# Performance work log

Measured on AMD Instinct MI355X. Metric: run time of the kernel, lower is better.

The kernel has to match this reference:

```python
import jax, jax.numpy as jnp
import numpy as np

B, L, N, CIN = 16, 12, 2048, 3
EMB, GRAP, LAYERS, OUT = 64, 16, 3, 12
SP, TID, DIW = 16, 16, 16
M = EMB + SP + TID + DIW  # model_size = 112


def setup_inputs() -> dict:
    key = jax.random.key(0)
    ks = jax.random.split(key, 12)
    s = jnp.float32(0.02)
    return {
        "history_data": jax.random.uniform(ks[0], (B, L, N, CIN), dtype=jnp.float32),
        "adj": jax.nn.softmax(jax.random.normal(ks[1], (N, N), dtype=jnp.float32), axis=1),
        "node_emb": jax.random.normal(ks[2], (N, SP), dtype=jnp.float32) * s,
        "tid_emb": jax.random.normal(ks[3], (288, TID), dtype=jnp.float32) * s,
        "diw_emb": jax.random.normal(ks[4], (7, DIW), dtype=jnp.float32) * s,
        "W_in": jax.random.normal(ks[5], (CIN, EMB), dtype=jnp.float32) * s,
        "b_in": jnp.zeros((EMB,), jnp.float32),
        "W_pre": jax.random.normal(ks[6], (M, 4 * M), dtype=jnp.float32) * s,
        "b_pre": jnp.zeros((4 * M,), jnp.float32),
        "E_dy": jax.random.normal(ks[7], (N, GRAP), dtype=jnp.float32) * s,
        "W_dy": jax.random.normal(ks[8], (M, 4 * M), dtype=jnp.float32) * s,
        "b_dy": jnp.zeros((4 * M,), jnp.float32),
        "W_dec": jax.random.normal(ks[9], (OUT, LAYERS, M), dtype=jnp.float32) * s,
        "b_dec": jnp.zeros((OUT,), jnp.float32),
        "W_out": jax.random.normal(ks[10], (OUT, OUT), dtype=jnp.float32) * s,
        "b_out": jnp.zeros((OUT,), jnp.float32),
    }


def _run_layer(hidd_t, A, W, b):
    """Graph-conv LSTM-style recurrent layer; returns last-timestep hidden [B,N,M]."""
    def step(ct, x):  # x: [B,N,M]
        xa = jnp.einsum('bkm,nk->bnm', x, A)      # adjacency message passing
        gates = xa @ W + b                         # [B,N,4M]
        i, f, g, o = jnp.split(gates, 4, axis=-1)
        ct = jax.nn.sigmoid(f) * ct + jax.nn.sigmoid(i) * jnp.tanh(g)
        ht = jax.nn.sigmoid(o) * jnp.tanh(ct)
        return ct, ht
    ct0 = jnp.zeros(hidd_t.shape[1:], hidd_t.dtype)  # [B,N,M]
    _, hts = jax.lax.scan(step, ct0, hidd_t)
    return hts[-1]


def reference(history_data, adj, node_emb, tid_emb, diw_emb, W_in, b_in,
              W_pre, b_pre, E_dy, W_dy, b_dy, W_dec, b_dec, W_out, b_out):
    Bx, Lx = history_data.shape[0], history_data.shape[1]
    # temporal embedding indices (truncating cast, matches torch LongTensor)
    t_idx = (history_data[..., 1] * 288).astype(jnp.int32)
    d_idx = (history_data[..., 2] * 7).astype(jnp.int32)
    inp = history_data @ W_in + b_in                                   # [B,L,N,EMB]
    node = jnp.broadcast_to(node_emb, (Bx, Lx) + node_emb.shape)       # [B,L,N,SP]
    hidd = jnp.concatenate([inp, node, tid_emb[t_idx], diw_emb[d_idx]], axis=-1)  # [B,L,N,M]
    hidd_t = jnp.moveaxis(hidd, 1, 0)                                  # [L,B,N,M]
    A_dy = jax.nn.softmax(jax.nn.relu(E_dy @ E_dy.T), axis=1)          # adaptive adjacency
    outs = [_run_layer(hidd_t, adj, W_pre, b_pre)]                     # layer 0: predefined graph
    for _ in range(LAYERS - 1):
        outs.append(_run_layer(hidd_t, A_dy, W_dy, b_dy))              # layers >0: dynamic graph
    final = jnp.stack(outs, axis=1)                                    # [B,LAYERS,N,M]
    # decoder Conv2d(layer_num->out_len, kernel (1,M)) then 1x1 Conv2d
    x = jnp.einsum('bznm,ozm->bon', final, W_dec) + b_dec[None, :, None]
    x = jnp.einsum('bon,po->bpn', x, W_out) + b_out[None, :, None]
    return x  # [B,OUT,N]
```

## Files before the change

### kernel.cpp

```cpp
#include <hip/hip_runtime.h>
#include <hip/hip_bf16.h>
#include <cstdint>
#include <cstddef>

typedef float f4 __attribute__((ext_vector_type(4)));
typedef short s16x8 __attribute__((ext_vector_type(8)));
typedef short s16x4 __attribute__((ext_vector_type(4)));

#define N_NODES 2048
#define BATCH 16
#define LSEQ 12
#define MDIM 112
#define GDIM 448
#define KC 35
#define NCOLS_X 6784
#define NREAL (KC*BATCH*LSEQ)
#define XROW 7680
#define KBIG 2048
#define KL 64
#define WTB_SH (GDIM * KL)

#define GLDS16(SRC, DST)                                                        \
    __builtin_amdgcn_global_load_lds(                                           \
        (const __attribute__((address_space(1))) void*)(SRC),                   \
        (__attribute__((address_space(3))) void*)(DST), 16, 0, 0)

#define MFMA16(ACC, AV, BV) \
    ACC = __builtin_amdgcn_mfma_f32_16x16x32_bf16(AV, BV, ACC, 0, 0, 0)

__device__ __forceinline__ short bf16hi(float v) {
    union { __hip_bfloat16 h; short s; } u;
    u.h = __float2bfloat16(v);
    return u.s;
}
__device__ __forceinline__ short bf16lo(float v) {
    union { __hip_bfloat16 h; short s; } u;
    u.h = __float2bfloat16(v);
    float r = v - __bfloat162float(u.h);
    u.h = __float2bfloat16(r);
    return u.s;
}
__device__ __forceinline__ float rcpf_(float x)  { return __builtin_amdgcn_rcpf(x); }
__device__ __forceinline__ float sigf_(float x)  { return rcpf_(1.0f + __expf(-x)); }
__device__ __forceinline__ float tanhf_(float x) { return 1.0f - 2.0f * rcpf_(1.0f + __expf(2.0f * x)); }

__device__ __forceinline__ float wave_sum(float v) {
#pragma unroll
    for (int off = 32; off > 0; off >>= 1) v += __shfl_down(v, off);
    return v;
}

__global__ void adaptive_adj_kernel(const float* __restrict__ E,
                                    const float* __restrict__ node_emb,
                                    __hip_bfloat16* __restrict__ Abig,
                                    float* __restrict__ node_a,
                                    float* __restrict__ rs)
{
    __shared__ float sbuf[N_NODES];
    __shared__ float red[256];
    __shared__ float part[17][4];
    const int n = blockIdx.x;
    const int tid = threadIdx.x;
    float en[16];
#pragma unroll
    for (int i = 0; i < 16; ++i) en[i] = E[n * 16 + i];
    float lmax = -3.4e38f;
    for (int k = tid; k < N_NODES; k += 256) {
        const float* ek = E + k * 16;
        float d = 0.f;
#pragma unroll
        for (int i = 0; i < 16; ++i) d += en[i] * ek[i];
        d = fmaxf(d, 0.0f);
        sbuf[k] = d;
        lmax = fmaxf(lmax, d);
    }
    red[tid] = lmax; __syncthreads();
    for (int s = 128; s > 0; s >>= 1) {
        if (tid < s) red[tid] = fmaxf(red[tid], red[tid + s]);
        __syncthreads();
    }
    float mx = red[0];
    __syncthreads();
    float lsum = 0.f;
    for (int k = tid; k < N_NODES; k += 256) {
        float e = __expf(sbuf[k] - mx);
        sbuf[k] = e;
        lsum += e;
    }
    red[tid] = lsum; __syncthreads();
    for (int s = 128; s > 0; s >>= 1) {
        if (tid < s) red[tid] += red[tid + s];
        __syncthreads();
    }
    float rinv = rcpf_(red[0]);
    __syncthreads();

    __hip_bfloat16* arow = Abig + (size_t)(2048 + n) * KBIG;
    float p[17];
#pragma unroll
    for (int i = 0; i < 17; ++i) p[i] = 0.f;
    for (int k = tid; k < N_NODES; k += 256) {
        float a = sbuf[k] * rinv;
        arow[k] = __float2bfloat16(a);
        const float* e = node_emb + k * 16;
        p[16] += a;
#pragma unroll
        for (int i = 0; i < 16; ++i) p[i] += a * e[i];
    }
#pragma unroll
    for (int e = 0; e < 17; ++e) {
        float v = wave_sum(p[e]);
        if ((tid & 63) == 0) part[e][tid >> 6] = v;
    }
    __syncthreads();
    if (tid < 17) {
        float s = part[tid][0] + part[tid][1] + part[tid][2] + part[tid][3];
        if (tid < 16) node_a[n * 16 + tid] = s;
        else rs[n] = s;
    }
}

__global__ void node_rs_kernel(const float* __restrict__ A,
                               const float* __restrict__ node_emb,
                               float* __restrict__ node_a, float* __restrict__ rs)
{
    __shared__ float part[17][4];
    const int n = blockIdx.x;
    const int tid = threadIdx.x;
    float p[17];
#pragma unroll
    for (int i = 0; i < 17; ++i) p[i] = 0.f;
    for (int k = tid; k < N_NODES; k += 256) {
        float a = A[(size_t)n * N_NODES + k];
        const float* e = node_emb + k * 16;
        p[16] += a;
#pragma unroll
        for (int i = 0; i < 16; ++i) p[i] += a * e[i];
    }
#pragma unroll
    for (int e = 0; e < 17; ++e) {
        float v = wave_sum(p[e]);
        if ((tid & 63) == 0) part[e][tid >> 6] = v;
    }
    __syncthreads();
    if (tid < 17) {
        float s = part[tid][0] + part[tid][1] + part[tid][2] + part[tid][3];
        if (tid < 16) node_a[n * 16 + tid] = s;
        else rs[n] = s;
    }
}

__global__ void wtb_pack_kernel(const float* __restrict__ W_in,
                                const float* __restrict__ b_in,
                                const float* __restrict__ Wp,
                                const float* __restrict__ bp,
                                const float* __restrict__ Wd,
                                const float* __restrict__ bd,
                                short* __restrict__ outp)
{
    int idx = blockIdx.x * 256 + threadIdx.x;
    if (idx >= 2 * GDIM * KL) return;
    int z = idx >= GDIM * KL;
    int rem = idx - z * GDIM * KL;
    const float* W  = z ? Wd : Wp;
    const float* bg = z ? bd : bp;
    int p = rem & 63;
    int r = rem >> 6;
    int tile = r >> 4, gc = r & 15;
    int mi = tile >> 2, co = tile & 3;
    int g = co * 112 + mi * 16 + gc;

    float v = 0.f; bool lo = false; bool zero = false;
    #define DOTW(VEC) ({ float s_ = 0.f;                                     \
        for (int m = 0; m < 64; ++m) s_ += (VEC)[m] * W[(size_t)m * GDIM + g];\
        s_; })
    if (p < 3)         v = DOTW(W_in + p * 64);
    else if (p < 35)   v = W[(size_t)(80 + p - 3) * GDIM + g];
    else if (p < 38)   v = DOTW(W_in + (p - 35) * 64);
    else if (p < 41) { v = DOTW(W_in + (p - 38) * 64); lo = true; }
    else if (p == 41)  v = bg[g];
    else if (p == 42)  v = DOTW(b_in);
    else if (p < 59)   v = W[(size_t)(64 + p - 43) * GDIM + g];
    else if (p == 59) { v = bg[g]; lo = true; }
    else if (p == 60) { v = DOTW(b_in); lo = true; }
    else zero = true;
    #undef DOTW
    short s = zero ? (short)0 : (lo ? bf16lo(v) : bf16hi(v));
    int a = r * 128 + p * 2;
    int asw = a ^ (((a >> 7) & 7) << 4);
    outp[(size_t)z * WTB_SH + (asw >> 1)] = s;
}

#define AQUADS (2048 * 2048 / 4)
#define XQUADS (NCOLS_X * 2048 / 4)
__global__ void pack_build_kernel(const float* __restrict__ adj,
                                  const float* __restrict__ hist,
                                  const float* __restrict__ tid_emb,
                                  const float* __restrict__ diw_emb,
                                  __hip_bfloat16* __restrict__ Abig,
                                  __hip_bfloat16* __restrict__ XT)
{
    int idx = blockIdx.x * 256 + threadIdx.x;
    if (idx < AQUADS) {
        int e0 = idx << 2;
        int k = e0 & 2047;
        int m = e0 >> 11;
        f4 v = *(const f4*)(adj + (size_t)m * 2048 + k);
        s16x4 o = { bf16hi(v[0]), bf16hi(v[1]), bf16hi(v[2]), bf16hi(v[3]) };
        *(s16x4*)((short*)Abig + (size_t)m * KBIG + k) = o;
        return;
    }
    int xi = idx - AQUADS;
    if (xi >= XQUADS) return;
    int e0 = xi << 2;
    int k0 = e0 & 2047;
    int jl = e0 >> 11;
    s16x4 o = {0, 0, 0, 0};
    if (jl < NREAL) {
        int c = jl % KC;
        int bl = jl / KC;
#pragma unroll
        for (int i = 0; i < 4; ++i) {
            const float* h = hist + ((size_t)(bl * N_NODES + k0 + i)) * 3;
            float v;
            if (c < 3) v = h[c];
            else if (c < 19) { int ti = (int)(h[1] * 288.0f); v = tid_emb[ti * 16 + (c - 3)]; }
            else             { int di = (int)(h[2] * 7.0f);   v = diw_emb[di * 16 + (c - 19)]; }
            o[i] = bf16hi(v);
        }
    }
    *(s16x4*)((short*)XT + (size_t)jl * KBIG + k0) = o;
}

__global__ __launch_bounds__(512, 4) void gemm_bf16_kernel(const short* __restrict__ A,
                                                           const short* __restrict__ BT,
                                                           short* __restrict__ XAhi)
{
    __shared__ short As[256 * 32];
    __shared__ short Bs[128 * 32];
    const int tid = threadIdx.x;
    const int w = tid >> 6;
    const int l = tid & 63;
    const int wr = w >> 1;
    const int wc = w & 1;

    const int bid = blockIdx.y * 53 + blockIdx.x;
    const int sid = (bid & 7) * 106 + (bid >> 3);
    const int col = sid >> 4;
    const int row = sid & 15;
    const int m0 = row * 256;
    const int jt = col * 128;

    const int arow0 = tid >> 2;
    const int akc   = (tid & 3) * 8;
    const size_t gA0 = (size_t)(m0 + arow0) * KBIG + akc;
    const size_t gA1 = (size_t)(m0 + 128 + arow0) * KBIG + akc;
    const size_t gB0 = (size_t)(jt + arow0) * KBIG + akc;
    char* lA0 = (char*)As + tid * 16;
    char* lA1 = (char*)As + 8192 + tid * 16;
    char* lB0 = (char*)Bs + tid * 16;

    f4 acc[4][4];
#pragma unroll
    for (int i = 0; i < 4; ++i)
#pragma unroll
        for (int j = 0; j < 4; ++j)
#pragma unroll
            for (int e = 0; e < 4; ++e) acc[i][j][e] = 0.f;

    const int fkof = (l >> 4) * 8;

    for (int kt = 0; kt < KBIG; kt += 32) {
        __syncthreads();
        GLDS16(A  + gA0 + kt, lA0);
        GLDS16(A  + gA1 + kt, lA1);
        GLDS16(BT + gB0 + kt, lB0);
        __syncthreads();
        s16x8 a[4], b[4];
#pragma unroll
        for (int mi = 0; mi < 4; ++mi)
            a[mi] = *(const s16x8*)&As[(wr * 64 + mi * 16 + (l & 15)) * 32 + fkof];
#pragma unroll
        for (int ni = 0; ni < 4; ++ni)
            b[ni] = *(const s16x8*)&Bs[(wc * 64 + ni * 16 + (l & 15)) * 32 + fkof];
#pragma unroll
        for (int mi = 0; mi < 4; ++mi)
#pragma unroll
            for (int ni = 0; ni < 4; ++ni)
                MFMA16(acc[mi][ni], a[mi], b[ni]);
    }

    const int rbase = m0 + wr * 64 + (l >> 4) * 4;
    const int cbase = jt + wc * 64 + (l & 15);
#pragma unroll
    for (int mi = 0; mi < 4; ++mi)
#pragma unroll
        for (int ni = 0; ni < 4; ++ni) {
            int cc = cbase + ni * 16;
            if (cc < NREAL) {
                int bt = cc / KC;
                int c  = cc - bt * KC;
#pragma unroll
                for (int reg = 0; reg < 4; ++reg) {
                    size_t roff = (size_t)(rbase + mi * 16 + reg) * XROW;
                    float v = acc[mi][ni][reg];
                    XAhi[roff + (size_t)bt * 40 + c] = bf16hi(v);
                    if (c < 3) XAhi[roff + (size_t)bt * 40 + 36 + c] = bf16lo(v);
                }
            }
        }
}

__global__ __launch_bounds__(512, 4) void lstm6_kernel(
    const short* __restrict__ XAhi,
    const short* __restrict__ WtBg,
    const float* __restrict__ na_pre, const float* __restrict__ na_dy,
    const float* __restrict__ rs_pre, const float* __restrict__ rs_dy,
    float* __restrict__ H)
{
    __shared__ short sWtb[WTB_SH];
    __shared__ short sXa[128 * KL];
    const int tid = threadIdx.x;
    const int w = tid >> 6, l = tid & 63;
    const int n0 = blockIdx.x * 128;
    const int b  = blockIdx.y;
    const int z  = blockIdx.z;
    const float* na = z ? na_dy : na_pre;
    const float* rs = z ? rs_dy : rs_pre;

    {
        const char* gW = (const char*)(WtBg + (size_t)z * WTB_SH);
        char* lW = (char*)sWtb;
        for (int it = 0; it < 7; ++it) {
            int base = (it * 8 + w) * 64;
            GLDS16(gW + (size_t)(base + l) * 16, lW + base * 16);
        }
    }

    const int sr = tid & 127;
    const int pp = tid >> 7;
    const short* xarow = XAhi + (size_t)(z * 2048 + n0 + sr) * XROW;
    const float* narow = na + (size_t)(n0 + sr) * 16;
    const float rsv = rs[n0 + sr];
    char* wrow = (char*)sXa + sr * 128;
    const int wswz = (sr & 7) << 4;

    const int lm = l & 15;
    const int sm = (l & 7) << 4;
    const int kof0 = ((l >> 4) * 16) ^ sm;
    const int kof1 = (64 + (l >> 4) * 16) ^ sm;
    const int an = w * 16 + lm;
    const char* xab = (const char*)sXa;
    const char* wtbb = (const char*)sWtb;
    float* Hout = H + (size_t)z * BATCH * N_NODES * MDIM;

    float cc[7][4];
#pragma unroll
    for (int mi = 0; mi < 7; ++mi)
#pragma unroll
        for (int q = 0; q < 4; ++q) cc[mi][q] = 0.f;

    s16x8 ph0 = {0,0,0,0,0,0,0,0}, ph1 = ph0;
    s16x4 p0 = {0,0,0,0}, p32 = p0, plo = p0;
    {
        const int bt = b * LSEQ;
        if (pp < 2) {
            ph0 = *(const s16x8*)(xarow + bt * 40 + pp * 16);
            ph1 = *(const s16x8*)(xarow + bt * 40 + pp * 16 + 8);
        } else if (pp == 2) {
            p0  = *(const s16x4*)(xarow + bt * 40);
            p32 = *(const s16x4*)(xarow + bt * 40 + 32);
            plo = *(const s16x4*)(xarow + bt * 40 + 36);
        }
    }

    for (int t = 0; t < LSEQ; ++t) {
        __syncthreads();
        if (pp < 2) {
            *(s16x8*)(wrow + ((pp * 32 + 0)  ^ wswz)) = ph0;
            *(s16x8*)(wrow + ((pp * 32 + 16) ^ wswz)) = ph1;
        } else if (pp == 2) {
            short v[16];
            v[0] = p32[0]; v[1] = p32[1]; v[2] = p32[2];
            v[3] = plo[0]; v[4] = plo[1]; v[5] = plo[2];
            v[6] = p0[0];  v[7] = p0[1];  v[8] = p0[2];
            v[9]  = bf16hi(1.0f);
            v[10] = bf16hi(rsv);
#pragma unroll
            for (int j = 11; j < 16; ++j) v[j] = bf16hi(narow[j - 11]);
#pragma unroll
            for (int q = 0; q < 4; ++q) {
                s16x4 sv = { v[q * 4], v[q * 4 + 1], v[q * 4 + 2], v[q * 4 + 3] };
                *(s16x4*)(wrow + ((2 * 32 + q * 8) ^ wswz)) = sv;
            }
        } else {
            short v[16];
#pragma unroll
            for (int j = 0; j < 11; ++j) v[j] = bf16hi(narow[5 + j]);
            v[11] = bf16hi(1.0f);
            v[12] = bf16hi(rsv);
            v[13] = 0; v[14] = 0; v[15] = 0;
#pragma unroll
            for (int q = 0; q < 4; ++q) {
                s16x4 sv = { v[q * 4], v[q * 4 + 1], v[q * 4 + 2], v[q * 4 + 3] };
                *(s16x4*)(wrow + ((3 * 32 + q * 8) ^ wswz)) = sv;
            }
        }
        __syncthreads();

        if (t + 1 < LSEQ) {
            const int bt = b * LSEQ + t + 1;
            if (pp < 2) {
                ph0 = *(const s16x8*)(xarow + bt * 40 + pp * 16);
                ph1 = *(const s16x8*)(xarow + bt * 40 + pp * 16 + 8);
            } else if (pp == 2) {
                p0  = *(const s16x4*)(xarow + bt * 40);
                p32 = *(const s16x4*)(xarow + bt * 40 + 32);
                plo = *(const s16x4*)(xarow + bt * 40 + 36);
            }
        }

        s16x8 a0 = *(const s16x8*)(xab + an * 128 + kof0);
        s16x8 a1 = *(const s16x8*)(xab + an * 128 + kof1);
#pragma unroll
        for (int mi = 0; mi < 7; ++mi) {
            const char* bb = wtbb + (mi * 64 + lm) * 128;
            f4 gi = {0.f, 0.f, 0.f, 0.f};
            f4 gf = gi, gg = gi;
            MFMA16(gi, a0, *(const s16x8*)(bb + kof0));
            MFMA16(gi, a1, *(const s16x8*)(bb + kof1));
            MFMA16(gf, a0, *(const s16x8*)(bb + 2048 + kof0));
            MFMA16(gf, a1, *(const s16x8*)(bb + 2048 + kof1));
            MFMA16(gg, a0, *(const s16x8*)(bb + 4096 + kof0));
            MFMA16(gg, a1, *(const s16x8*)(bb + 4096 + kof1));
#pragma unroll
            for (int q = 0; q < 4; ++q) {
                float si = sigf_(gi[q]);
                float sf = sigf_(gf[q]);
                float tg = tanhf_(gg[q]);
                cc[mi][q] = sf * cc[mi][q] + si * tg;
            }
            if (t == LSEQ - 1) {
                f4 go = {0.f, 0.f, 0.f, 0.f};
                MFMA16(go, a0, *(const s16x8*)(bb + 6144 + kof0));
                MFMA16(go, a1, *(const s16x8*)(bb + 6144 + kof1));
#pragma unroll
                for (int q = 0; q < 4; ++q) {
                    float h = sigf_(go[q]) * tanhf_(cc[mi][q]);
                    Hout[((size_t)b * N_NODES + n0 + w * 16 + (l >> 4) * 4 + q) * MDIM
                         + mi * 16 + lm] = h;
                }
            }
        }
    }
}

__global__ void decode_kernel(const float* __restrict__ H,
                              const float* __restrict__ Wdec,
                              const float* __restrict__ bdec,
                              const float* __restrict__ Wout,
                              const float* __restrict__ bout,
                              float* __restrict__ out)
{
    int g = blockIdx.x * 256 + threadIdx.x;
    if (g >= BATCH * N_NODES) return;
    int b = g >> 11;
    int n = g & 2047;
    const f4* h0 = (const f4*)(H + (size_t)g * MDIM);
    const f4* h1 = (const f4*)(H + (size_t)BATCH * N_NODES * MDIM + (size_t)g * MDIM);
    float x[12];
#pragma unroll
    for (int o = 0; o < 12; ++o) x[o] = bdec[o];
    for (int mq = 0; mq < 28; ++mq) {
        f4 a0 = h0[mq], a1 = h1[mq];
#pragma unroll
        for (int e = 0; e < 4; ++e) {
            int m = mq * 4 + e;
#pragma unroll
            for (int o = 0; o < 12; ++o)
                x[o] += a0[e] * Wdec[(o * 3 + 0) * MDIM + m]
                      + a1[e] * (Wdec[(o * 3 + 1) * MDIM + m] + Wdec[(o * 3 + 2) * MDIM + m]);
        }
    }
#pragma unroll
    for (int p = 0; p < 12; ++p) {
        float s = bout[p];
#pragma unroll
        for (int o = 0; o < 12; ++o) s += Wout[p * 12 + o] * x[o];
        out[((size_t)b * 12 + p) * N_NODES + n] = s;
    }
}

extern "C" void kernel_launch(void* const* d_in, const int* in_sizes, int n_in,
                              void* d_out, int out_size, void* d_ws, size_t ws_size,
                              hipStream_t stream)
{
    const float* hist   = (const float*)d_in[0];
    const float* adj    = (const float*)d_in[1];
    const float* node_e = (const float*)d_in[2];
    const float* tid_e  = (const float*)d_in[3];
    const float* diw_e  = (const float*)d_in[4];
    const float* W_in   = (const float*)d_in[5];
    const float* b_in   = (const float*)d_in[6];
    const float* W_pre  = (const float*)d_in[7];
    const float* b_pre  = (const float*)d_in[8];
    const float* E_dy   = (const float*)d_in[9];
    const float* W_dy   = (const float*)d_in[10];
    const float* b_dy   = (const float*)d_in[11];
    const float* W_dec  = (const float*)d_in[12];
    const float* b_dec  = (const float*)d_in[13];
    const float* W_out  = (const float*)d_in[14];
    const float* b_out  = (const float*)d_in[15];
    float* out = (float*)d_out;

    float* ws = (float*)d_ws;
    const size_t XAHI_F = (size_t)4096 * XROW / 2;
    const size_t ABIG_F = (size_t)4096 * KBIG / 2;
    const size_t XT_F   = (size_t)NCOLS_X * KBIG / 2;

    short* XAhi  = (short*)ws;
    float* AbigF = ws + XAHI_F;
    __hip_bfloat16* Abig = (__hip_bfloat16*)AbigF;
    float* H     = AbigF;
    __hip_bfloat16* XTc = (__hip_bfloat16*)(ws + XAHI_F + ABIG_F);
    float* tail = ws + XAHI_F + ABIG_F + XT_F;
    float* na_pre = tail;                     tail += (size_t)N_NODES * 16;
    float* na_dy  = tail;                     tail += (size_t)N_NODES * 16;
    float* rs_pre = tail;                     tail += N_NODES;
    float* rs_dy  = tail;                     tail += N_NODES;
    short* WtBg   = (short*)tail;

    adaptive_adj_kernel<<<N_NODES, 256, 0, stream>>>(E_dy, node_e, Abig, na_dy, rs_dy);
    node_rs_kernel<<<N_NODES, 256, 0, stream>>>(adj, node_e, na_pre, rs_pre);
    wtb_pack_kernel<<<(2 * GDIM * KL + 255) / 256, 256, 0, stream>>>(
        W_in, b_in, W_pre, b_pre, W_dy, b_dy, WtBg);

    pack_build_kernel<<<(AQUADS + XQUADS + 255) / 256, 256, 0, stream>>>(
        adj, hist, tid_e, diw_e, Abig, XTc);

    gemm_bf16_kernel<<<dim3(53, 16), 512, 0, stream>>>(
        (const short*)Abig, (const short*)XTc, XAhi);

    lstm6_kernel<<<dim3(N_NODES / 128, BATCH, 2), 512, 0, stream>>>(
        XAhi, WtBg, na_pre, na_dy, rs_pre, rs_dy, H);

    decode_kernel<<<(BATCH * N_NODES + 255) / 256, 256, 0, stream>>>(
        H, W_dec, b_dec, W_out, b_out, out);
}
```

Measured before the change: 348.4 us.

## Double GEMM K-tile to 64 with XOR-swizzled LDS layout

```diff
diff --git a/kernel.cpp b/kernel.cpp
--- a/kernel.cpp
+++ b/kernel.cpp
@@ -236,13 +236,14 @@
                                                            const short* __restrict__ BT,
                                                            short* __restrict__ XAhi)
 {
-    __shared__ short As[256 * 32];
-    __shared__ short Bs[128 * 32];
+    __shared__ short As[256 * 64];
+    __shared__ short Bs[128 * 64];
     const int tid = threadIdx.x;
     const int w = tid >> 6;
     const int l = tid & 63;
     const int wr = w >> 1;
     const int wc = w & 1;
+    const int lm = l & 15;
 
     const int bid = blockIdx.y * 53 + blockIdx.x;
     const int sid = (bid & 7) * 106 + (bid >> 3);
@@ -251,14 +252,12 @@
     const int m0 = row * 256;
     const int jt = col * 128;
 
-    const int arow0 = tid >> 2;
-    const int akc   = (tid & 3) * 8;
-    const size_t gA0 = (size_t)(m0 + arow0) * KBIG + akc;
-    const size_t gA1 = (size_t)(m0 + 128 + arow0) * KBIG + akc;
-    const size_t gB0 = (size_t)(jt + arow0) * KBIG + akc;
-    char* lA0 = (char*)As + tid * 16;
-    char* lA1 = (char*)As + 8192 + tid * 16;
-    char* lB0 = (char*)Bs + tid * 16;
+    const int srow = tid >> 3;
+    const int koct = (tid & 7) ^ (srow & 7);
+    const size_t gA = (size_t)(m0 + srow) * KBIG + koct * 8;
+    const size_t gB = (size_t)(jt + srow) * KBIG + koct * 8;
+    char* lA = (char*)As + srow * 128 + (tid & 7) * 16;
+    char* lB = (char*)Bs + srow * 128 + (tid & 7) * 16;
 
     f4 acc[4][4];
 #pragma unroll
@@ -268,30 +267,38 @@
 #pragma unroll
             for (int e = 0; e < 4; ++e) acc[i][j][e] = 0.f;
 
-    const int fkof = (l >> 4) * 8;
-
-    for (int kt = 0; kt < KBIG; kt += 32) {
+    const int sm  = (l & 7) << 4;
+    const int k16 = (l >> 4) * 16;
+
+    for (int kt = 0; kt < KBIG; kt += 64) {
         __syncthreads();
-        GLDS16(A  + gA0 + kt, lA0);
-        GLDS16(A  + gA1 + kt, lA1);
-        GLDS16(BT + gB0 + kt, lB0);
+        GLDS16(A  + gA + kt,                      lA);
+        GLDS16(A  + gA + kt + (size_t)64  * KBIG, lA + 64  * 128);
+        GLDS16(A  + gA + kt + (size_t)128 * KBIG, lA + 128 * 128);
+        GLDS16(A  + gA + kt + (size_t)192 * KBIG, lA + 192 * 128);
+        GLDS16(BT + gB + kt,                      lB);
+        GLDS16(BT + gB + kt + (size_t)64  * KBIG, lB + 64  * 128);
         __syncthreads();
-        s16x8 a[4], b[4];
-#pragma unroll
-        for (int mi = 0; mi < 4; ++mi)
-            a[mi] = *(const s16x8*)&As[(wr * 64 + mi * 16 + (l & 15)) * 32 + fkof];
-#pragma unroll
-        for (int ni = 0; ni < 4; ++ni)
-            b[ni] = *(const s16x8*)&Bs[(wc * 64 + ni * 16 + (l & 15)) * 32 + fkof];
-#pragma unroll
-        for (int mi = 0; mi < 4; ++mi)
+#pragma unroll
+        for (int ks = 0; ks < 2; ++ks) {
+            const int ko = (ks * 64 + k16) ^ sm;
+            s16x8 a[4], b[4];
+#pragma unroll
+            for (int mi = 0; mi < 4; ++mi)
+                a[mi] = *(const s16x8*)((const char*)As + (wr * 64 + mi * 16 + lm) * 128 + ko);
 #pragma unroll
             for (int ni = 0; ni < 4; ++ni)
-                MFMA16(acc[mi][ni], a[mi], b[ni]);
+                b[ni] = *(const s16x8*)((const char*)Bs + (wc * 64 + ni * 16 + lm) * 128 + ko);
+#pragma unroll
+            for (int mi = 0; mi < 4; ++mi)
+#pragma unroll
+                for (int ni = 0; ni < 4; ++ni)
+                    MFMA16(acc[mi][ni], a[mi], b[ni]);
+        }
     }
 
     const int rbase = m0 + wr * 64 + (l >> 4) * 4;
-    const int cbase = jt + wc * 64 + (l & 15);
+    const int cbase = jt + wc * 64 + lm;
 #pragma unroll
     for (int mi = 0; mi < 4; ++mi)
 #pragma unroll
```

After: 319.0 us. 8.4% less time.
